# Kernel tuning notes

Hardware: AMD Instinct MI355X
Metric: run time of the kernel (lower is better)

Reference implementation:

```python
import jax, jax.numpy as jnp
import numpy as np

BN_EPS = 1e-5
POOL_EPS = 1e-6


def conv3x3(x, w, b):
    # x: (N,C,H,W), w: (O,C,3,3) -> (N,O,H,W), stride 1, SAME padding
    y = jax.lax.conv_general_dilated(x, w, window_strides=(1, 1), padding='SAME',
                                     dimension_numbers=('NCHW', 'OIHW', 'NCHW'))
    return y + b[None, :, None, None]


def deform_conv2d(x, off_w, off_b, mod_w, mod_b, w, b):
    # Modulated deformable conv (DCNv2), 3x3, stride 1, padding 1 (torchvision semantics).
    N, C, H, W = x.shape
    off = conv3x3(x, off_w, off_b).reshape(N, 9, 2, H, W)  # per-tap (dy, dx)
    mod = 2.0 * jax.nn.sigmoid(conv3x3(x, mod_w, mod_b))   # (N,9,H,W)
    dy = (jnp.arange(3, dtype=x.dtype) - 1.0).repeat(3)    # tap k = ky*3+kx
    dx = jnp.tile(jnp.arange(3, dtype=x.dtype) - 1.0, 3)
    py = off[:, :, 0] + dy[None, :, None, None] + jnp.arange(H, dtype=x.dtype)[None, None, :, None]
    px = off[:, :, 1] + dx[None, :, None, None] + jnp.arange(W, dtype=x.dtype)[None, None, None, :]
    y0f = jnp.floor(py); x0f = jnp.floor(px)
    wy = py - y0f; wx = px - x0f
    y0 = y0f.astype(jnp.int32); x0 = x0f.astype(jnp.int32)
    flat = x.reshape(N, C, H * W)

    def gather(yi, xi):
        # zero padding outside the image
        valid = ((yi >= 0) & (yi < H) & (xi >= 0) & (xi < W)).astype(x.dtype)
        idx = jnp.clip(yi, 0, H - 1) * W + jnp.clip(xi, 0, W - 1)      # (N,9,H,W)
        idx_b = jnp.broadcast_to(idx.reshape(N, 1, -1), (N, C, 9 * H * W))
        g = jnp.take_along_axis(flat, idx_b, axis=2).reshape(N, C, 9, H, W)
        return g * valid[:, None]

    s = (gather(y0, x0) * ((1 - wy) * (1 - wx))[:, None]
         + gather(y0, x0 + 1) * ((1 - wy) * wx)[:, None]
         + gather(y0 + 1, x0) * (wy * (1 - wx))[:, None]
         + gather(y0 + 1, x0 + 1) * (wy * wx)[:, None])       # (N,C,9,H,W)
    out = jnp.einsum('nckij,nkij,ock->noij', s, mod, w.reshape(w.shape[0], C, 9))
    return out + b[None, :, None, None]


def setup_inputs() -> dict:
    key = jax.random.key(0)
    ks = jax.random.split(key, 20)
    b, n_f, n_i, Hm, Wm = 2, 8, 10, 192, 192
    C_in, C_dcn, n_inc, n_pix = 256, 64, 128, 64
    h, w = 96, 96
    f32 = jnp.float32
    inp = {
        'x': jax.random.normal(ks[0], (b * n_f, C_in, h, w), f32),
        'masks': jax.random.uniform(ks[1], (b, n_f, n_i, Hm, Wm), f32),
        'conv1_w': jax.random.normal(ks[2], (C_dcn, C_in, 3, 3), f32) * 0.02,
        'conv1_b': jnp.zeros((C_dcn,), f32),
        'bn_gamma': jnp.ones((C_dcn,), f32),
        'bn_beta': jnp.zeros((C_dcn,), f32),
        'bn_mean': jax.random.normal(ks[3], (C_dcn,), f32) * 0.01,
        'bn_var': jnp.ones((C_dcn,), f32),
        'off_w': jax.random.normal(ks[4], (18, C_dcn, 3, 3), f32) * 0.01,
        'off_b': jnp.zeros((18,), f32),
        'mod_w': jax.random.normal(ks[5], (9, C_dcn, 3, 3), f32) * 0.01,
        'mod_b': jnp.zeros((9,), f32),
        'dcn_w': jax.random.normal(ks[6], (C_dcn, C_dcn, 3, 3), f32) * 0.05,
        'dcn_b': jnp.zeros((C_dcn,), f32),
        'smooth_w': jax.random.normal(ks[7], (C_dcn, C_dcn), f32) * 0.05,
        'smooth_b': jnp.zeros((C_dcn,), f32),
        'inc_w': jax.random.normal(ks[8], (n_inc, C_dcn), f32) * 0.05,
        'pix_w': jax.random.normal(ks[9], (n_pix, C_dcn), f32) * 0.05,
    }
    return inp


def reference(x, masks, conv1_w, conv1_b, bn_gamma, bn_beta, bn_mean, bn_var,
              off_w, off_b, mod_w, mod_b, dcn_w, dcn_b,
              smooth_w, smooth_b, inc_w, pix_w):
    # conv1: Conv3x3 + BatchNorm (eval stats) + ReLU
    y = conv3x3(x, conv1_w, conv1_b)
    y = (y - bn_mean[None, :, None, None]) * (bn_gamma[None, :, None, None]
        * jax.lax.rsqrt(bn_var + BN_EPS)[None, :, None, None]) + bn_beta[None, :, None, None]
    y = jax.nn.relu(y)
    # deformable conv
    y = deform_conv2d(y, off_w, off_b, mod_w, mod_b, dcn_w, dcn_b)

    b, n_f, n_i, Hm, Wm = masks.shape
    N, C, h, w = y.shape
    # resizeAnyShape -> bilinear, align_corners=False
    m = jax.image.resize(masks.reshape(b * n_f * n_i, Hm, Wm),
                         (b * n_f * n_i, h, w), method='bilinear', antialias=False)
    m = m.reshape(b, n_f, n_i, h * w)
    xf = y.reshape(b, n_f, C, h * w)
    # mask-weighted spatial average: avoid (b,n_f,n_i,C,h*w) intermediate
    num = jnp.einsum('bfcp,bfip->bfic', xf, m)            # (b,n_f,n_i,C)
    den = m.sum(axis=-1)[..., None]                        # (b,n_f,n_i,1)
    feat = num / (den + POOL_EPS)
    feat = jax.nn.relu(feat @ smooth_w.T + smooth_b)
    inc_kernels = feat @ inc_w.T
    pix_kernels = feat @ pix_w.T
    return (inc_kernels, pix_kernels)
```

## Files before the change

kernel.cpp:

```cpp
#include <hip/hip_runtime.h>
#include <hip/hip_bf16.h>

typedef __attribute__((ext_vector_type(8))) __bf16 bf16x8;
typedef __attribute__((ext_vector_type(4))) float f32x4;
typedef __attribute__((ext_vector_type(2))) float f32x2;
typedef __attribute__((ext_vector_type(4))) unsigned int u32x4;
typedef __attribute__((ext_vector_type(2))) unsigned int u32x2;
typedef __attribute__((ext_vector_type(4))) unsigned short u16x4;
typedef __attribute__((ext_vector_type(8))) unsigned short ushort8;

#define MFMA16(a,b,c) __builtin_amdgcn_mfma_f32_16x16x32_bf16((a),(b),(c),0,0,0)

__device__ __forceinline__ float b2f(unsigned short u) {
  union { unsigned int i; float f; } v; v.i = ((unsigned int)u) << 16; return v.f;
}
__device__ __forceinline__ unsigned short f2b(float f) {
  union { float f; unsigned int u; } v; v.f = f;
  unsigned int u = v.u;
  unsigned int r = (u + 0x7fffu + ((u >> 16) & 1u)) >> 16;
  return (unsigned short)r;
}
__device__ __forceinline__ unsigned short f2h(float f) {
  _Float16 x = (_Float16)f; unsigned short r; __builtin_memcpy(&r, &x, 2); return r;
}
__device__ __forceinline__ float h2f(unsigned short h) {
  _Float16 x; __builtin_memcpy(&x, &h, 2); return (float)x;
}

#define NIMG 16
#define CIN  256
#define CD   64
#define HH   96
#define WW   96
#define HW   (HH*WW)

#define OFF_Y1   (0ll)
#define OFF_Y2   (18874368ll)
#define OFF_OFF  (37748736ll)
#define OFF_MOD  (48365568ll)
#define OFF_M    (53673984ll)
#define OFF_NP   OFF_OFF
#define OFF_DP   (OFF_OFF + 2621440ll)
#define OFF_SBN  (59908096ll)
#define OFF_TBN  (59908352ll)
#define OFF_W1   (59908608ll)
#define OFF_W2   (60203520ll)
#define OFF_W3   (60240384ll)
#define WS_NEEDED (60314112ll)

__global__ void k_prep(const float* __restrict__ conv1_w, const float* __restrict__ conv1_b,
                       const float* __restrict__ bn_gamma, const float* __restrict__ bn_beta,
                       const float* __restrict__ bn_mean, const float* __restrict__ bn_var,
                       const float* __restrict__ off_w, const float* __restrict__ mod_w,
                       const float* __restrict__ dcn_w,
                       unsigned short* __restrict__ w1, unsigned short* __restrict__ w2,
                       unsigned short* __restrict__ w3,
                       float* __restrict__ sbn, float* __restrict__ tbn)
{
  int e = blockIdx.x * 256 + threadIdx.x;
  if (e < 147456) {
    int j = e & 7, o = (e >> 3) & 63, cg = (e >> 9) & 31, t = e >> 14;
    w1[e] = f2b(conv1_w[(o * 256 + cg * 8 + j) * 9 + t]);
  } else if (e < 147456 + 18432) {
    int i = e - 147456;
    int j = i & 7, o = (i >> 3) & 31, cg = (i >> 8) & 7, t = i >> 11;
    int ch = cg * 8 + j;
    float v = 0.f;
    if (o < 18)      v = off_w[(o * 64 + ch) * 9 + t];
    else if (o < 27) v = mod_w[((o - 18) * 64 + ch) * 9 + t];
    w2[i] = f2b(v);
  } else if (e < 147456 + 18432 + 36864) {
    int i = e - 147456 - 18432;
    int j = i & 7, o = (i >> 3) & 63, cg = (i >> 9) & 7, t = i >> 12;
    w3[i] = f2b(dcn_w[(o * 64 + cg * 8 + j) * 9 + t]);
  } else {
    int i = e - (147456 + 18432 + 36864);
    if (i < 64) {
      sbn[i] = bn_gamma[i] * rsqrtf(bn_var[i] + 1e-5f);
    } else if (i < 128) {
      int q = i - 64;
      float s = bn_gamma[q] * rsqrtf(bn_var[q] + 1e-5f);
      tbn[q] = (conv1_b[q] - bn_mean[q]) * s + bn_beta[q];
    }
  }
}

__global__ __launch_bounds__(256)
void k_tr(const float* __restrict__ x, unsigned short* __restrict__ xT, int n_base)
{
  __shared__ __align__(16) unsigned short ls[64][68];
  const int tid = threadIdx.x;
  const int p0 = blockIdx.x * 64, c0 = blockIdx.y * 64, nl = blockIdx.z;
  const float* xn = x + (size_t)(n_base + nl) * CIN * HW;

  const int p4 = tid & 15, cb = tid >> 4;
  #pragma unroll
  for (int it = 0; it < 4; ++it) {
    int c = cb + it * 16;
    f32x4 v = *reinterpret_cast<const f32x4*>(xn + (size_t)(c0 + c) * HW + p0 + p4 * 4);
    #pragma unroll
    for (int q = 0; q < 4; ++q) ls[p4 * 4 + q][c] = f2b(v[q]);
  }
  __syncthreads();
  const int cg = tid & 7, pb = tid >> 3;
  #pragma unroll
  for (int it = 0; it < 2; ++it) {
    int p = pb + it * 32;
    u32x2 lo = *reinterpret_cast<const u32x2*>(&ls[p][cg * 8]);
    u32x2 hi = *reinterpret_cast<const u32x2*>(&ls[p][cg * 8 + 4]);
    u32x4 v = {lo[0], lo[1], hi[0], hi[1]};
    *reinterpret_cast<u32x4*>(&xT[((size_t)nl * HW + p0 + p) * CIN + c0 + cg * 8]) = v;
  }
}

__global__ __launch_bounds__(256)
void k_conv1t(const unsigned short* __restrict__ xT, const unsigned short* __restrict__ w1,
              const float* __restrict__ sbn, const float* __restrict__ tbn,
              unsigned short* __restrict__ y1, int n_base)
{
  __shared__ __align__(16) unsigned short sbuf[3 * 98 * 40];
  #define XS(r,w,c) sbuf[((r) * 98 + (w)) * 40 + (c)]

  const int tid = threadIdx.x;
  const int lane = tid & 63, wv = tid >> 6;
  const int l16 = lane & 15, lg = lane >> 4;
  const int wch = wv & 1, wpx = wv >> 1;
  const int h = blockIdx.x;
  const int nl = blockIdx.y;
  const int n = n_base + nl;
  const unsigned short* xn = xT + (size_t)nl * HW * CIN;

  f32x4 acc[2][3];
  #pragma unroll
  for (int a = 0; a < 2; ++a)
    #pragma unroll
    for (int b = 0; b < 3; ++b) { f32x4 z = {0.f,0.f,0.f,0.f}; acc[a][b] = z; }

  for (int chunk = 0; chunk < 8; ++chunk) {
    const int c0 = chunk * 32;
    __syncthreads();
    #pragma unroll
    for (int it = 0; it < 5; ++it) {
      int idx = tid + it * 256;
      if (idx < 1152) {
        int cg = idx & 3, w = (idx >> 2) % 96, r = idx / 384;
        int row = h - 1 + r;
        u32x4 v = {0u,0u,0u,0u};
        if (row >= 0 && row < HH)
          v = *reinterpret_cast<const u32x4*>(&xn[((size_t)row * WW + w) * CIN + c0 + cg * 8]);
        *reinterpret_cast<u32x4*>(&XS(r, w + 1, cg * 8)) = v;
      }
    }
    if (tid < 24) {
      int r = tid >> 3, side = (tid >> 2) & 1, cg = tid & 3;
      u32x4 z = {0u,0u,0u,0u};
      *reinterpret_cast<u32x4*>(&XS(r, side * 97, cg * 8)) = z;
    }
    __syncthreads();
    #pragma unroll
    for (int t = 0; t < 9; ++t) {
      const int ky = t / 3, kx = t % 3;
      bf16x8 a0 = *reinterpret_cast<const bf16x8*>(
          &w1[((t * 32 + chunk * 4 + lg) * 64 + wch * 32 + l16) * 8]);
      bf16x8 a1 = *reinterpret_cast<const bf16x8*>(
          &w1[((t * 32 + chunk * 4 + lg) * 64 + wch * 32 + 16 + l16) * 8]);
      #pragma unroll
      for (int wt = 0; wt < 3; ++wt) {
        bf16x8 b = *reinterpret_cast<const bf16x8*>(&XS(ky, wpx*48 + wt*16 + l16 + kx, lg*8));
        acc[0][wt] = MFMA16(a0, b, acc[0][wt]);
        acc[1][wt] = MFMA16(a1, b, acc[1][wt]);
      }
    }
  }
  __syncthreads();
  unsigned short* ys = &sbuf[0];
  #pragma unroll
  for (int ct = 0; ct < 2; ++ct) {
    int o4 = wch * 32 + ct * 16 + lg * 4;
    f32x4 s4 = *reinterpret_cast<const f32x4*>(&sbn[o4]);
    f32x4 t4 = *reinterpret_cast<const f32x4*>(&tbn[o4]);
    #pragma unroll
    for (int wt = 0; wt < 3; ++wt) {
      int p = wpx * 48 + wt * 16 + l16;
      float v0 = acc[ct][wt][0] * s4[0] + t4[0]; v0 = v0 > 0.f ? v0 : 0.f;
      float v1 = acc[ct][wt][1] * s4[1] + t4[1]; v1 = v1 > 0.f ? v1 : 0.f;
      float v2 = acc[ct][wt][2] * s4[2] + t4[2]; v2 = v2 > 0.f ? v2 : 0.f;
      float v3 = acc[ct][wt][3] * s4[3] + t4[3]; v3 = v3 > 0.f ? v3 : 0.f;
      u32x2 d = {(unsigned)f2b(v0) | ((unsigned)f2b(v1) << 16),
                 (unsigned)f2b(v2) | ((unsigned)f2b(v3) << 16)};
      *reinterpret_cast<u32x2*>(&ys[p * 72 + o4]) = d;
    }
  }
  __syncthreads();
  #pragma unroll
  for (int it = 0; it < 3; ++it) {
    int idx = tid + it * 256;
    int cg = idx & 7, p = idx >> 3;
    *reinterpret_cast<u32x4*>(&y1[(((size_t)n * HH + h) * WW + p) * CD + cg * 8]) =
      *reinterpret_cast<const u32x4*>(&ys[p * 72 + cg * 8]);
  }
  #undef XS
}

__global__ __launch_bounds__(256)
void k_conv2(const unsigned short* __restrict__ y1, const unsigned short* __restrict__ w2,
             const float* __restrict__ off_b, const float* __restrict__ mod_b,
             float* __restrict__ off_o, float* __restrict__ mod_o)
{
  __shared__ __align__(16) unsigned short xs[4][98][40];

  const int tid = threadIdx.x;
  const int lane = tid & 63, wv = tid >> 6;
  const int l16 = lane & 15, lg = lane >> 4;
  const int wrow = wv & 1, wct = wv >> 1;
  const int h0 = blockIdx.x * 2;
  const int n = blockIdx.y;
  const unsigned short* y1n = y1 + (size_t)n * HW * CD;

  f32x4 acc[6];
  #pragma unroll
  for (int b = 0; b < 6; ++b) { f32x4 z = {0.f,0.f,0.f,0.f}; acc[b] = z; }

  #pragma unroll
  for (int chunk = 0; chunk < 2; ++chunk) {
    const int c0 = chunk * 32;
    bf16x8 aR[9];
    #pragma unroll
    for (int t = 0; t < 9; ++t)
      aR[t] = *reinterpret_cast<const bf16x8*>(
          &w2[((t * 8 + chunk * 4 + lg) * 32 + wct * 16 + l16) * 8]);
    __syncthreads();
    #pragma unroll
    for (int it = 0; it < 6; ++it) {
      int idx = tid + it * 256;
      int cg = idx & 3, w = (idx >> 2) % 96, r = idx / 384;
      int row = h0 - 1 + r;
      u32x4 v = {0u,0u,0u,0u};
      if (row >= 0 && row < HH)
        v = *reinterpret_cast<const u32x4*>(&y1n[((size_t)row * WW + w) * CD + c0 + cg * 8]);
      *reinterpret_cast<u32x4*>(&xs[r][w + 1][cg * 8]) = v;
    }
    if (tid < 32) {
      int r = tid >> 3, side = (tid >> 2) & 1, cg = tid & 3;
      u32x4 z = {0u,0u,0u,0u};
      *reinterpret_cast<u32x4*>(&xs[r][side * 97][cg * 8]) = z;
    }
    __syncthreads();
    #pragma unroll
    for (int t = 0; t < 9; ++t) {
      const int ky = t / 3, kx = t % 3;
      const int r = wrow + ky;
      #pragma unroll
      for (int wt = 0; wt < 6; ++wt) {
        bf16x8 b = *reinterpret_cast<const bf16x8*>(&xs[r][wt*16 + l16 + kx][lg*8]);
        acc[wt] = MFMA16(aR[t], b, acc[wt]);
      }
    }
  }
  const int h = h0 + wrow;
  #pragma unroll
  for (int j = 0; j < 4; ++j) {
    int o = wct * 16 + lg * 4 + j;
    if (o < 18) {
      float bo = off_b[o];
      #pragma unroll
      for (int wt = 0; wt < 6; ++wt)
        off_o[((n * 18 + o) * HH + h) * WW + wt * 16 + l16] = acc[wt][j] + bo;
    } else if (o < 27) {
      int q = o - 18;
      float bo = mod_b[q];
      #pragma unroll
      for (int wt = 0; wt < 6; ++wt) {
        float v = acc[wt][j] + bo;
        mod_o[((n * 9 + q) * HH + h) * WW + wt * 16 + l16] = 2.f / (1.f + expf(-v));
      }
    }
  }
}

__global__ __launch_bounds__(256)
void k_dcn(const unsigned short* __restrict__ y1, const float* __restrict__ off_i,
           const float* __restrict__ mod_i, const unsigned short* __restrict__ w3g,
           const float* __restrict__ dcn_b, unsigned short* __restrict__ y2)
{
  __shared__ __align__(16) unsigned short meta[864][8];
  __shared__ __align__(16) unsigned short Bs[96][72];

  const int tid = threadIdx.x;
  const int lane = tid & 63, wv = tid >> 6;
  const int l16 = lane & 15, lg = lane >> 4;
  const int h = blockIdx.x, n = blockIdx.y;

  #pragma unroll
  for (int it = 0; it < 4; ++it) {
    int e = tid + it * 256;
    if (e < 864) {
      int k = e / 96, p = e % 96;
      float dy = off_i[((n * 18 + 2 * k) * HH + h) * WW + p];
      float dx = off_i[((n * 18 + 2 * k + 1) * HH + h) * WW + p];
      float mw = mod_i[((n * 9 + k) * HH + h) * WW + p];
      float py = (float)(h + k / 3 - 1) + dy;
      float px = (float)(p + k % 3 - 1) + dx;
      float y0f = floorf(py), x0f = floorf(px);
      float wy = py - y0f, wx = px - x0f;
      int iy0 = (int)y0f, ix0 = (int)x0f;
      int iy1 = iy0 + 1, ix1 = ix0 + 1;
      float vy0 = (iy0 >= 0 && iy0 < HH) ? 1.f : 0.f;
      float vy1 = (iy1 >= 0 && iy1 < HH) ? 1.f : 0.f;
      float vx0 = (ix0 >= 0 && ix0 < WW) ? 1.f : 0.f;
      float vx1 = (ix1 >= 0 && ix1 < WW) ? 1.f : 0.f;
      unsigned short m0 = f2h((1.f - wy) * (1.f - wx) * mw * vy0 * vx0);
      unsigned short m1 = f2h((1.f - wy) * wx         * mw * vy0 * vx1);
      unsigned short m2 = f2h(wy         * (1.f - wx) * mw * vy1 * vx0);
      unsigned short m3 = f2h(wy         * wx         * mw * vy1 * vx1);
      int cy0 = iy0 < 0 ? 0 : (iy0 > 95 ? 95 : iy0);
      int cy1 = iy1 < 0 ? 0 : (iy1 > 95 ? 95 : iy1);
      int cx0 = ix0 < 0 ? 0 : (ix0 > 95 ? 95 : ix0);
      int cx1 = ix1 < 0 ? 0 : (ix1 > 95 ? 95 : ix1);
      u32x4 pk = {(unsigned)m0 | ((unsigned)m1 << 16),
                  (unsigned)m2 | ((unsigned)m3 << 16),
                  (unsigned)(cy0 * WW + cx0) | ((unsigned)(cy0 * WW + cx1) << 16),
                  (unsigned)(cy1 * WW + cx0) | ((unsigned)(cy1 * WW + cx1) << 16)};
      *reinterpret_cast<u32x4*>(&meta[e][0]) = pk;
    }
  }
  __syncthreads();

  const unsigned short* y1n = y1 + (size_t)n * HW * CD;
  f32x4 acc[6];
  #pragma unroll
  for (int b = 0; b < 6; ++b) { f32x4 z = {0.f,0.f,0.f,0.f}; acc[b] = z; }

  #pragma unroll
  for (int t = 0; t < 9; ++t) {
    bf16x8 a0 = *reinterpret_cast<const bf16x8*>(
        &w3g[((t * 8 + lg) * 64 + wv * 16 + l16) * 8]);
    bf16x8 a1 = *reinterpret_cast<const bf16x8*>(
        &w3g[((t * 8 + 4 + lg) * 64 + wv * 16 + l16) * 8]);
    #pragma unroll
    for (int it = 0; it < 3; ++it) {
      int idx = tid + it * 256;
      int cg = idx & 7, p = idx >> 3;
      u32x4 mk = *reinterpret_cast<const u32x4*>(&meta[t * 96 + p][0]);
      float hw0 = h2f((unsigned short)(mk[0] & 0xffffu));
      float hw1 = h2f((unsigned short)(mk[0] >> 16));
      float hw2 = h2f((unsigned short)(mk[1] & 0xffffu));
      float hw3 = h2f((unsigned short)(mk[1] >> 16));
      int o0 = (int)(mk[2] & 0xffffu) << 6;
      int o1 = (int)(mk[2] >> 16) << 6;
      int o2 = (int)(mk[3] & 0xffffu) << 6;
      int o3 = (int)(mk[3] >> 16) << 6;
      ushort8 g0 = *reinterpret_cast<const ushort8*>(&y1n[o0 + cg * 8]);
      ushort8 g1 = *reinterpret_cast<const ushort8*>(&y1n[o1 + cg * 8]);
      ushort8 g2 = *reinterpret_cast<const ushort8*>(&y1n[o2 + cg * 8]);
      ushort8 g3 = *reinterpret_cast<const ushort8*>(&y1n[o3 + cg * 8]);
      unsigned int wds[4];
      #pragma unroll
      for (int q = 0; q < 4; ++q) {
        float va = hw0*b2f(g0[2*q])   + hw1*b2f(g1[2*q])
                 + hw2*b2f(g2[2*q])   + hw3*b2f(g3[2*q]);
        float vb = hw0*b2f(g0[2*q+1]) + hw1*b2f(g1[2*q+1])
                 + hw2*b2f(g2[2*q+1]) + hw3*b2f(g3[2*q+1]);
        wds[q] = (unsigned int)f2b(va) | ((unsigned int)f2b(vb) << 16);
      }
      u32x4 pk = {wds[0], wds[1], wds[2], wds[3]};
      *reinterpret_cast<u32x4*>(&Bs[p][cg * 8]) = pk;
    }
    __syncthreads();
    #pragma unroll
    for (int wt = 0; wt < 6; ++wt) {
      bf16x8 b0 = *reinterpret_cast<const bf16x8*>(&Bs[wt * 16 + l16][lg * 8]);
      bf16x8 b1 = *reinterpret_cast<const bf16x8*>(&Bs[wt * 16 + l16][32 + lg * 8]);
      acc[wt] = MFMA16(a0, b0, acc[wt]);
      acc[wt] = MFMA16(a1, b1, acc[wt]);
    }
    __syncthreads();
  }

  unsigned short* Bs2 = &Bs[0][0];
  {
    int o4 = wv * 16 + lg * 4;
    f32x4 b4 = *reinterpret_cast<const f32x4*>(&dcn_b[o4]);
    #pragma unroll
    for (int wt = 0; wt < 6; ++wt) {
      int p = wt * 16 + l16;
      u32x2 d = {(unsigned)f2b(acc[wt][0] + b4[0]) | ((unsigned)f2b(acc[wt][1] + b4[1]) << 16),
                 (unsigned)f2b(acc[wt][2] + b4[2]) | ((unsigned)f2b(acc[wt][3] + b4[3]) << 16)};
      *reinterpret_cast<u32x2*>(&Bs2[p * 72 + o4]) = d;
    }
  }
  __syncthreads();
  #pragma unroll
  for (int it = 0; it < 3; ++it) {
    int idx = tid + it * 256;
    int cg = idx & 7, p = idx >> 3;
    *reinterpret_cast<u32x4*>(&y2[(((size_t)n * HH + h) * WW + p) * CD + cg * 8]) =
      *reinterpret_cast<const u32x4*>(&Bs2[p * 72 + cg * 8]);
  }
}

__global__ void k_resize(const float* __restrict__ masks, float* __restrict__ m)
{
  int gid = blockIdx.x * 256 + threadIdx.x;
  if (gid >= 16 * 10 * HH * 48) return;
  int ow2 = (gid % 48) * 2;
  int oh = (gid / 48) % HH;
  int r = gid / (48 * HH);
  const float* s = masks + ((size_t)r * 192 + 2 * oh) * 192 + 2 * ow2;
  f32x4 v0 = *reinterpret_cast<const f32x4*>(s);
  f32x4 v1 = *reinterpret_cast<const f32x4*>(s + 192);
  f32x2 o = {0.25f * (v0[0] + v0[1] + v1[0] + v1[1]),
             0.25f * (v0[2] + v0[3] + v1[2] + v1[3])};
  *reinterpret_cast<f32x2*>(&m[(size_t)r * HW + oh * WW + ow2]) = o;
}

__global__ __launch_bounds__(256)
void k_pool(const unsigned short* __restrict__ y2, const float* __restrict__ m,
            float* __restrict__ num_part, float* __restrict__ den_part)
{
  __shared__ float ms2[144][12];
  __shared__ float red[4][10][64];
  __shared__ float den_red[10][16];
  const int tid = threadIdx.x;
  const int seg = blockIdx.x, bf = blockIdx.y;
  const int p0 = seg * 144;

  #pragma unroll
  for (int it = 0; it < 6; ++it) {
    int idx = tid + it * 256;
    if (idx < 1440) {
      int i = idx / 144, p = idx % 144;
      ms2[p][i] = m[(bf * 10 + i) * HW + p0 + p];
    }
  }
  __syncthreads();

  const int c = tid & 63, grp = tid >> 6;
  f32x2 acc2[5];
  #pragma unroll
  for (int i = 0; i < 5; ++i) { f32x2 z = {0.f, 0.f}; acc2[i] = z; }
  const unsigned short* yb = y2 + ((size_t)bf * HW + p0 + grp * 36) * CD + c;
  for (int p = 0; p < 36; ++p) {
    float v = b2f(yb[p * CD]);
    f32x2 vv = {v, v};
    int pp = grp * 36 + p;
    #pragma unroll
    for (int i2 = 0; i2 < 5; ++i2) {
      f32x2 mp = *reinterpret_cast<const f32x2*>(&ms2[pp][i2 * 2]);
      acc2[i2] += vv * mp;
    }
  }
  #pragma unroll
  for (int i2 = 0; i2 < 5; ++i2) {
    red[grp][2 * i2 + 0][c] = acc2[i2][0];
    red[grp][2 * i2 + 1][c] = acc2[i2][1];
  }
  if (tid < 160) {
    int i = tid >> 4, s16 = tid & 15;
    float s = 0.f;
    for (int k2 = 0; k2 < 9; ++k2) s += ms2[s16 + k2 * 16][i];
    den_red[i][s16] = s;
  }
  __syncthreads();
  #pragma unroll
  for (int it = 0; it < 3; ++it) {
    int e = tid + it * 256;
    if (e < 640) {
      int i = e >> 6, cc = e & 63;
      num_part[((bf * 64 + seg) * 10 + i) * 64 + cc] =
        red[0][i][cc] + red[1][i][cc] + red[2][i][cc] + red[3][i][cc];
    }
  }
  if (tid < 10) {
    float s = 0.f;
    for (int k2 = 0; k2 < 16; ++k2) s += den_red[tid][k2];
    den_part[(bf * 64 + seg) * 16 + tid] = s;
  }
}

__global__ void k_head(const float* __restrict__ num_part, const float* __restrict__ den_part,
                       const float* __restrict__ smooth_w, const float* __restrict__ smooth_b,
                       const float* __restrict__ inc_w, const float* __restrict__ pix_w,
                       float* __restrict__ out)
{
  __shared__ float pool_s[10][64];
  __shared__ float feat_s[10][64];
  const int tid = threadIdx.x;
  const int bf = blockIdx.x;
  #pragma unroll
  for (int it = 0; it < 3; ++it) {
    int e = tid + it * 256;
    if (e < 640) {
      int i = e >> 6, cc = e & 63;
      float nsum = 0.f, dsum = 0.f;
      for (int s = 0; s < 64; ++s) {
        nsum += num_part[((bf * 64 + s) * 10 + i) * 64 + cc];
        dsum += den_part[(bf * 64 + s) * 16 + i];
      }
      pool_s[i][cc] = nsum / (dsum + 1e-6f);
    }
  }
  __syncthreads();
  #pragma unroll
  for (int it = 0; it < 3; ++it) {
    int e = tid + it * 256;
    if (e < 640) {
      int i = e >> 6, cc = e & 63;
      float s = smooth_b[cc];
      for (int k = 0; k < 64; ++k) s += pool_s[i][k] * smooth_w[cc * 64 + k];
      feat_s[i][cc] = s > 0.f ? s : 0.f;
    }
  }
  __syncthreads();
  #pragma unroll
  for (int it = 0; it < 5; ++it) {
    int e = tid + it * 256;
    if (e < 1280) {
      int i = e >> 7, oc = e & 127;
      float s = 0.f;
      for (int k = 0; k < 64; ++k) s += feat_s[i][k] * inc_w[oc * 64 + k];
      out[(bf * 10 + i) * 128 + oc] = s;
    }
  }
  #pragma unroll
  for (int it = 0; it < 3; ++it) {
    int e = tid + it * 256;
    if (e < 640) {
      int i = e >> 6, oc = e & 63;
      float s = 0.f;
      for (int k = 0; k < 64; ++k) s += feat_s[i][k] * pix_w[oc * 64 + k];
      out[20480 + (bf * 10 + i) * 64 + oc] = s;
    }
  }
}

extern "C" void kernel_launch(void* const* d_in, const int* in_sizes, int n_in,
                              void* d_out, int out_size, void* d_ws, size_t ws_size,
                              hipStream_t stream)
{
  const float* x        = (const float*)d_in[0];
  const float* masks    = (const float*)d_in[1];
  const float* conv1_w  = (const float*)d_in[2];
  const float* conv1_b  = (const float*)d_in[3];
  const float* bn_gamma = (const float*)d_in[4];
  const float* bn_beta  = (const float*)d_in[5];
  const float* bn_mean  = (const float*)d_in[6];
  const float* bn_var   = (const float*)d_in[7];
  const float* off_w    = (const float*)d_in[8];
  const float* off_b    = (const float*)d_in[9];
  const float* mod_w    = (const float*)d_in[10];
  const float* mod_b    = (const float*)d_in[11];
  const float* dcn_w    = (const float*)d_in[12];
  const float* dcn_b    = (const float*)d_in[13];
  const float* smooth_w = (const float*)d_in[14];
  const float* smooth_b = (const float*)d_in[15];
  const float* inc_w    = (const float*)d_in[16];
  const float* pix_w    = (const float*)d_in[17];
  float* out = (float*)d_out;

  if (ws_size < (size_t)WS_NEEDED) return;
  char* ws = (char*)d_ws;
  unsigned short* y1  = (unsigned short*)(ws + OFF_Y1);
  unsigned short* y2  = (unsigned short*)(ws + OFF_Y2);
  unsigned short* xT  = (unsigned short*)(ws + OFF_Y2);
  float* off_t        = (float*)(ws + OFF_OFF);
  float* mod_t        = (float*)(ws + OFF_MOD);
  float* mbuf         = (float*)(ws + OFF_M);
  float* num_part     = (float*)(ws + OFF_NP);
  float* den_part     = (float*)(ws + OFF_DP);
  float* sbn          = (float*)(ws + OFF_SBN);
  float* tbn          = (float*)(ws + OFF_TBN);
  unsigned short* w1  = (unsigned short*)(ws + OFF_W1);
  unsigned short* w2  = (unsigned short*)(ws + OFF_W2);
  unsigned short* w3  = (unsigned short*)(ws + OFF_W3);

  k_prep<<<793, 256, 0, stream>>>(conv1_w, conv1_b, bn_gamma, bn_beta, bn_mean, bn_var,
                                  off_w, mod_w, dcn_w, w1, w2, w3, sbn, tbn);
  for (int pass = 0; pass < 2; ++pass) {
    int n_base = pass * 8;
    k_tr<<<dim3(144, 4, 8), 256, 0, stream>>>(x, xT, n_base);
    k_conv1t<<<dim3(96, 8), 256, 0, stream>>>(xT, w1, sbn, tbn, y1, n_base);
  }
  k_conv2<<<dim3(48, 16), 256, 0, stream>>>(y1, w2, off_b, mod_b, off_t, mod_t);
  k_dcn<<<dim3(96, 16), 256, 0, stream>>>(y1, off_t, mod_t, w3, dcn_b, y2);
  k_resize<<<(16 * 10 * HH * 48 + 255) / 256, 256, 0, stream>>>(masks, mbuf);
  k_pool<<<dim3(64, 16), 256, 0, stream>>>(y2, mbuf, num_part, den_part);
  k_head<<<16, 256, 0, stream>>>(num_part, den_part, smooth_w, smooth_b, inc_w, pix_w, out);
}
```

Baseline: 478.4 us.

## Restructure deformable conv to build MFMA B operands in registers

The deformable conv kernel now tiles 128 flattened pixels per block instead of one image row. Each wave gathers and bilinearly blends its own pixels directly into MFMA B-operand registers, which removes the shared-memory staging buffer and the two barriers per tap. Each wave also now covers all 64 output channels, so it loads 8 weight fragments per tap. Sampling weights are stored in shared memory as fp32 rather than fp16, and bf16 rounding uses the hardware conversion. The cost is more registers and more weight loads per wave, which may lower occupancy.

```diff
diff --git a/kernel.cpp b/kernel.cpp
--- a/kernel.cpp
+++ b/kernel.cpp
@@ -15,16 +15,10 @@
   union { unsigned int i; float f; } v; v.i = ((unsigned int)u) << 16; return v.f;
 }
 __device__ __forceinline__ unsigned short f2b(float f) {
-  union { float f; unsigned int u; } v; v.f = f;
-  unsigned int u = v.u;
-  unsigned int r = (u + 0x7fffu + ((u >> 16) & 1u)) >> 16;
-  return (unsigned short)r;
-}
-__device__ __forceinline__ unsigned short f2h(float f) {
-  _Float16 x = (_Float16)f; unsigned short r; __builtin_memcpy(&r, &x, 2); return r;
-}
-__device__ __forceinline__ float h2f(unsigned short h) {
-  _Float16 x; __builtin_memcpy(&x, &h, 2); return (float)x;
+  __bf16 h = (__bf16)f; unsigned short r; __builtin_memcpy(&r, &h, 2); return r;
+}
+__device__ __forceinline__ unsigned int pk2(float a, float b) {
+  return (unsigned int)f2b(a) | ((unsigned int)f2b(b) << 16);
 }
 
 #define NIMG 16
@@ -186,8 +180,7 @@
       float v1 = acc[ct][wt][1] * s4[1] + t4[1]; v1 = v1 > 0.f ? v1 : 0.f;
       float v2 = acc[ct][wt][2] * s4[2] + t4[2]; v2 = v2 > 0.f ? v2 : 0.f;
       float v3 = acc[ct][wt][3] * s4[3] + t4[3]; v3 = v3 > 0.f ? v3 : 0.f;
-      u32x2 d = {(unsigned)f2b(v0) | ((unsigned)f2b(v1) << 16),
-                 (unsigned)f2b(v2) | ((unsigned)f2b(v3) << 16)};
+      u32x2 d = {pk2(v0, v1), pk2(v2, v3)};
       *reinterpret_cast<u32x2*>(&ys[p * 72 + o4]) = d;
     }
   }
@@ -283,24 +276,28 @@
            const float* __restrict__ mod_i, const unsigned short* __restrict__ w3g,
            const float* __restrict__ dcn_b, unsigned short* __restrict__ y2)
 {
-  __shared__ __align__(16) unsigned short meta[864][8];
-  __shared__ __align__(16) unsigned short Bs[96][72];
+  __shared__ __align__(16) unsigned char smem[27648];
+  f32x4* wgt = reinterpret_cast<f32x4*>(smem);
+  u32x2* ofs = reinterpret_cast<u32x2*>(smem + 18432);
 
   const int tid = threadIdx.x;
   const int lane = tid & 63, wv = tid >> 6;
   const int l16 = lane & 15, lg = lane >> 4;
-  const int h = blockIdx.x, n = blockIdx.y;
-
-  #pragma unroll
-  for (int it = 0; it < 4; ++it) {
+  const int n = blockIdx.y;
+  const int p0 = blockIdx.x * 128;
+
+  #pragma unroll
+  for (int it = 0; it < 5; ++it) {
     int e = tid + it * 256;
-    if (e < 864) {
-      int k = e / 96, p = e % 96;
-      float dy = off_i[((n * 18 + 2 * k) * HH + h) * WW + p];
-      float dx = off_i[((n * 18 + 2 * k + 1) * HH + h) * WW + p];
-      float mw = mod_i[((n * 9 + k) * HH + h) * WW + p];
+    if (e < 1152) {
+      int k = e >> 7, pl = e & 127;
+      int p = p0 + pl;
+      int h = p / WW, w = p - h * WW;
+      float dy = off_i[(n * 18 + 2 * k) * HW + p];
+      float dx = off_i[(n * 18 + 2 * k + 1) * HW + p];
+      float mw = mod_i[(n * 9 + k) * HW + p];
       float py = (float)(h + k / 3 - 1) + dy;
-      float px = (float)(p + k % 3 - 1) + dx;
+      float px = (float)(w + k % 3 - 1) + dx;
       float y0f = floorf(py), x0f = floorf(px);
       float wy = py - y0f, wx = px - x0f;
       int iy0 = (int)y0f, ix0 = (int)x0f;
@@ -309,93 +306,104 @@
       float vy1 = (iy1 >= 0 && iy1 < HH) ? 1.f : 0.f;
       float vx0 = (ix0 >= 0 && ix0 < WW) ? 1.f : 0.f;
       float vx1 = (ix1 >= 0 && ix1 < WW) ? 1.f : 0.f;
-      unsigned short m0 = f2h((1.f - wy) * (1.f - wx) * mw * vy0 * vx0);
-      unsigned short m1 = f2h((1.f - wy) * wx         * mw * vy0 * vx1);
-      unsigned short m2 = f2h(wy         * (1.f - wx) * mw * vy1 * vx0);
-      unsigned short m3 = f2h(wy         * wx         * mw * vy1 * vx1);
+      f32x4 w4;
+      w4[0] = (1.f - wy) * (1.f - wx) * mw * vy0 * vx0;
+      w4[1] = (1.f - wy) * wx         * mw * vy0 * vx1;
+      w4[2] = wy         * (1.f - wx) * mw * vy1 * vx0;
+      w4[3] = wy         * wx         * mw * vy1 * vx1;
       int cy0 = iy0 < 0 ? 0 : (iy0 > 95 ? 95 : iy0);
       int cy1 = iy1 < 0 ? 0 : (iy1 > 95 ? 95 : iy1);
       int cx0 = ix0 < 0 ? 0 : (ix0 > 95 ? 95 : ix0);
       int cx1 = ix1 < 0 ? 0 : (ix1 > 95 ? 95 : ix1);
-      u32x4 pk = {(unsigned)m0 | ((unsigned)m1 << 16),
-                  (unsigned)m2 | ((unsigned)m3 << 16),
-                  (unsigned)(cy0 * WW + cx0) | ((unsigned)(cy0 * WW + cx1) << 16),
+      wgt[e] = w4;
+      u32x2 o2 = {(unsigned)(cy0 * WW + cx0) | ((unsigned)(cy0 * WW + cx1) << 16),
                   (unsigned)(cy1 * WW + cx0) | ((unsigned)(cy1 * WW + cx1) << 16)};
-      *reinterpret_cast<u32x4*>(&meta[e][0]) = pk;
+      ofs[e] = o2;
     }
   }
   __syncthreads();
 
   const unsigned short* y1n = y1 + (size_t)n * HW * CD;
-  f32x4 acc[6];
-  #pragma unroll
-  for (int b = 0; b < 6; ++b) { f32x4 z = {0.f,0.f,0.f,0.f}; acc[b] = z; }
-
-  #pragma unroll
+  f32x4 acc[4][2];
+  #pragma unroll
+  for (int a = 0; a < 4; ++a)
+    #pragma unroll
+    for (int b = 0; b < 2; ++b) { f32x4 z = {0.f,0.f,0.f,0.f}; acc[a][b] = z; }
+
+  const int lg8 = lg * 8;
+  #pragma unroll 1
   for (int t = 0; t < 9; ++t) {
-    bf16x8 a0 = *reinterpret_cast<const bf16x8*>(
-        &w3g[((t * 8 + lg) * 64 + wv * 16 + l16) * 8]);
-    bf16x8 a1 = *reinterpret_cast<const bf16x8*>(
-        &w3g[((t * 8 + 4 + lg) * 64 + wv * 16 + l16) * 8]);
-    #pragma unroll
-    for (int it = 0; it < 3; ++it) {
-      int idx = tid + it * 256;
-      int cg = idx & 7, p = idx >> 3;
-      u32x4 mk = *reinterpret_cast<const u32x4*>(&meta[t * 96 + p][0]);
-      float hw0 = h2f((unsigned short)(mk[0] & 0xffffu));
-      float hw1 = h2f((unsigned short)(mk[0] >> 16));
-      float hw2 = h2f((unsigned short)(mk[1] & 0xffffu));
-      float hw3 = h2f((unsigned short)(mk[1] >> 16));
-      int o0 = (int)(mk[2] & 0xffffu) << 6;
-      int o1 = (int)(mk[2] >> 16) << 6;
-      int o2 = (int)(mk[3] & 0xffffu) << 6;
-      int o3 = (int)(mk[3] >> 16) << 6;
-      ushort8 g0 = *reinterpret_cast<const ushort8*>(&y1n[o0 + cg * 8]);
-      ushort8 g1 = *reinterpret_cast<const ushort8*>(&y1n[o1 + cg * 8]);
-      ushort8 g2 = *reinterpret_cast<const ushort8*>(&y1n[o2 + cg * 8]);
-      ushort8 g3 = *reinterpret_cast<const ushort8*>(&y1n[o3 + cg * 8]);
-      unsigned int wds[4];
+    bf16x8 a[4][2];
+    #pragma unroll
+    for (int oct = 0; oct < 4; ++oct)
+      #pragma unroll
+      for (int kk = 0; kk < 2; ++kk)
+        a[oct][kk] = *reinterpret_cast<const bf16x8*>(
+            &w3g[((t * 8 + kk * 4 + lg) * 64 + oct * 16 + l16) * 8]);
+    #pragma unroll
+    for (int pxt = 0; pxt < 2; ++pxt) {
+      int pl = wv * 32 + pxt * 16 + l16;
+      f32x4 w4 = wgt[t * 128 + pl];
+      u32x2 o2 = ofs[t * 128 + pl];
+      const unsigned short* c0p = y1n + ((o2[0] & 0xffffu) << 6) + lg8;
+      const unsigned short* c1p = y1n + ((o2[0] >> 16) << 6) + lg8;
+      const unsigned short* c2p = y1n + ((o2[1] & 0xffffu) << 6) + lg8;
+      const unsigned short* c3p = y1n + ((o2[1] >> 16) << 6) + lg8;
+      ushort8 gA0 = *reinterpret_cast<const ushort8*>(c0p);
+      ushort8 gA1 = *reinterpret_cast<const ushort8*>(c1p);
+      ushort8 gA2 = *reinterpret_cast<const ushort8*>(c2p);
+      ushort8 gA3 = *reinterpret_cast<const ushort8*>(c3p);
+      ushort8 gB0 = *reinterpret_cast<const ushort8*>(c0p + 32);
+      ushort8 gB1 = *reinterpret_cast<const ushort8*>(c1p + 32);
+      ushort8 gB2 = *reinterpret_cast<const ushort8*>(c2p + 32);
+      ushort8 gB3 = *reinterpret_cast<const ushort8*>(c3p + 32);
+      unsigned int wa[4], wb[4];
       #pragma unroll
       for (int q = 0; q < 4; ++q) {
-        float va = hw0*b2f(g0[2*q])   + hw1*b2f(g1[2*q])
-                 + hw2*b2f(g2[2*q])   + hw3*b2f(g3[2*q]);
-        float vb = hw0*b2f(g0[2*q+1]) + hw1*b2f(g1[2*q+1])
-                 + hw2*b2f(g2[2*q+1]) + hw3*b2f(g3[2*q+1]);
-        wds[q] = (unsigned int)f2b(va) | ((unsigned int)f2b(vb) << 16);
-      }
-      u32x4 pk = {wds[0], wds[1], wds[2], wds[3]};
-      *reinterpret_cast<u32x4*>(&Bs[p][cg * 8]) = pk;
-    }
-    __syncthreads();
-    #pragma unroll
-    for (int wt = 0; wt < 6; ++wt) {
-      bf16x8 b0 = *reinterpret_cast<const bf16x8*>(&Bs[wt * 16 + l16][lg * 8]);
-      bf16x8 b1 = *reinterpret_cast<const bf16x8*>(&Bs[wt * 16 + l16][32 + lg * 8]);
-      acc[wt] = MFMA16(a0, b0, acc[wt]);
-      acc[wt] = MFMA16(a1, b1, acc[wt]);
-    }
-    __syncthreads();
-  }
-
-  unsigned short* Bs2 = &Bs[0][0];
-  {
-    int o4 = wv * 16 + lg * 4;
+        float a0 = w4[0]*b2f(gA0[2*q])   + w4[1]*b2f(gA1[2*q])
+                 + w4[2]*b2f(gA2[2*q])   + w4[3]*b2f(gA3[2*q]);
+        float a1 = w4[0]*b2f(gA0[2*q+1]) + w4[1]*b2f(gA1[2*q+1])
+                 + w4[2]*b2f(gA2[2*q+1]) + w4[3]*b2f(gA3[2*q+1]);
+        float b0 = w4[0]*b2f(gB0[2*q])   + w4[1]*b2f(gB1[2*q])
+                 + w4[2]*b2f(gB2[2*q])   + w4[3]*b2f(gB3[2*q]);
+        float b1 = w4[0]*b2f(gB0[2*q+1]) + w4[1]*b2f(gB1[2*q+1])
+                 + w4[2]*b2f(gB2[2*q+1]) + w4[3]*b2f(gB3[2*q+1]);
+        wa[q] = pk2(a0, a1);
+        wb[q] = pk2(b0, b1);
+      }
+      u32x4 ta = {wa[0], wa[1], wa[2], wa[3]};
+      u32x4 tb = {wb[0], wb[1], wb[2], wb[3]};
+      bf16x8 bfa = __builtin_bit_cast(bf16x8, ta);
+      bf16x8 bfb = __builtin_bit_cast(bf16x8, tb);
+      #pragma unroll
+      for (int oct = 0; oct < 4; ++oct) {
+        acc[oct][pxt] = MFMA16(a[oct][0], bfa, acc[oct][pxt]);
+        acc[oct][pxt] = MFMA16(a[oct][1], bfb, acc[oct][pxt]);
+      }
+    }
+  }
+
+  __syncthreads();
+  unsigned short* ys = reinterpret_cast<unsigned short*>(smem);
+  #pragma unroll
+  for (int oct = 0; oct < 4; ++oct) {
+    int o4 = oct * 16 + lg * 4;
     f32x4 b4 = *reinterpret_cast<const f32x4*>(&dcn_b[o4]);
     #pragma unroll
-    for (int wt = 0; wt < 6; ++wt) {
-      int p = wt * 16 + l16;
-      u32x2 d = {(unsigned)f2b(acc[wt][0] + b4[0]) | ((unsigned)f2b(acc[wt][1] + b4[1]) << 16),
-                 (unsigned)f2b(acc[wt][2] + b4[2]) | ((unsigned)f2b(acc[wt][3] + b4[3]) << 16)};
-      *reinterpret_cast<u32x2*>(&Bs2[p * 72 + o4]) = d;
-    }
-  }
-  __syncthreads();
-  #pragma unroll
-  for (int it = 0; it < 3; ++it) {
+    for (int pxt = 0; pxt < 2; ++pxt) {
+      int pl = wv * 32 + pxt * 16 + l16;
+      u32x2 d = {pk2(acc[oct][pxt][0] + b4[0], acc[oct][pxt][1] + b4[1]),
+                 pk2(acc[oct][pxt][2] + b4[2], acc[oct][pxt][3] + b4[3])};
+      *reinterpret_cast<u32x2*>(&ys[pl * 72 + o4]) = d;
+    }
+  }
+  __syncthreads();
+  #pragma unroll
+  for (int it = 0; it < 4; ++it) {
     int idx = tid + it * 256;
     int cg = idx & 7, p = idx >> 3;
-    *reinterpret_cast<u32x4*>(&y2[(((size_t)n * HH + h) * WW + p) * CD + cg * 8]) =
-      *reinterpret_cast<const u32x4*>(&Bs2[p * 72 + cg * 8]);
+    *reinterpret_cast<u32x4*>(&y2[((size_t)n * HW + p0 + p) * CD + cg * 8]) =
+      *reinterpret_cast<const u32x4*>(&ys[p * 72 + cg * 8]);
   }
 }
 
@@ -582,7 +590,7 @@
     k_conv1t<<<dim3(96, 8), 256, 0, stream>>>(xT, w1, sbn, tbn, y1, n_base);
   }
   k_conv2<<<dim3(48, 16), 256, 0, stream>>>(y1, w2, off_b, mod_b, off_t, mod_t);
-  k_dcn<<<dim3(96, 16), 256, 0, stream>>>(y1, off_t, mod_t, w3, dcn_b, y2);
+  k_dcn<<<dim3(72, 16), 256, 0, stream>>>(y1, off_t, mod_t, w3, dcn_b, y2);
   k_resize<<<(16 * 10 * HH * 48 + 255) / 256, 256, 0, stream>>>(masks, mbuf);
   k_pool<<<dim3(64, 16), 256, 0, stream>>>(y2, mbuf, num_part, den_part);
   k_head<<<16, 256, 0, stream>>>(num_part, den_part, smooth_w, smooth_b, inc_w, pix_w, out);
```

Result: slower. 501.1 us (+4.7%).
